# Performance work log

Hardware: AMD Instinct MI355X
Metric: run time of the kernel (lower is better)

## Reference

```python
import jax, jax.numpy as jnp
import numpy as np
import math

# Static configuration (matches init_kwargs / input_specs)
L1 = 2          # lmax of x
L2 = 2          # lmax of y
LZ = L1 + L2    # output lmax = 4
RB = 20         # res_beta (Gauss-Legendre nodes)
RA = 19         # res_alpha (uniform azimuthal samples)
MUL = 128       # input multiplicity per l
C = 128         # num_channels
N = 1024        # batch (nodes/edges)


def _assoc_legendre(l, m, x):
    """Associated Legendre P_l^m(x) with Condon-Shortley phase, via recurrence."""
    pmm = np.ones_like(x)
    if m > 0:
        dfact = float(np.prod(np.arange(1, 2 * m, 2)))  # (2m-1)!!
        pmm = ((-1.0) ** m) * dfact * (1.0 - x * x) ** (m / 2.0)
    if l == m:
        return pmm
    pmmp1 = x * (2 * m + 1) * pmm
    if l == m + 1:
        return pmmp1
    for ll in range(m + 2, l + 1):
        p = ((2 * ll - 1) * x * pmmp1 - (ll + m - 1) * pmm) / (ll - m)
        pmm, pmmp1 = pmmp1, p
    return pmmp1


def _sh_table(L, rb, ra):
    """Orthonormal real spherical harmonics sampled on the (beta, alpha) grid.

    Returns Y [(L+1)^2, rb, ra] and Gauss-Legendre weights qw [rb] such that
    sum_{b,a} f(b,a) Y_lm(b,a) qw[b] * (2*pi/ra) == c_lm exactly for
    bandlimited f (the inverse of the synthesis c -> grid).
    """
    ct, qw = np.polynomial.legendre.leggauss(rb)  # nodes = cos(beta)
    alpha = 2.0 * np.pi * np.arange(ra) / ra
    Y = np.zeros(((L + 1) ** 2, rb, ra))
    for l in range(L + 1):
        for m in range(-l, l + 1):
            am = abs(m)
            nlm = math.sqrt((2 * l + 1) / (4 * math.pi)
                            * math.factorial(l - am) / math.factorial(l + am))
            P = _assoc_legendre(l, am, ct)  # [rb]
            if m == 0:
                ang = np.ones(ra)
            elif m > 0:
                ang = math.sqrt(2.0) * np.cos(m * alpha)
            else:
                ang = math.sqrt(2.0) * np.sin(am * alpha)
            Y[l * l + l + m] = nlm * P[:, None] * ang[None, :]
    return Y, qw


_Y_np, _QW_np = _sh_table(LZ, RB, RA)
Y_TAB = jnp.asarray(_Y_np, jnp.float32)   # [(LZ+1)^2, RB, RA]
QW = jnp.asarray(_QW_np, jnp.float32)     # [RB]


def _per_l_linear_in(v, w, L):
    """Equivariant per-l linear: v [N, mul, (L+1)^2], w [L+1, mul, C] -> [N, C, (L+1)^2]."""
    scale = 1.0 / math.sqrt(v.shape[1])
    outs = [jnp.einsum('nmd,mc->ncd', v[..., l * l:(l + 1) ** 2], w[l]) * scale
            for l in range(L + 1)]
    return jnp.concatenate(outs, axis=-1)


def setup_inputs() -> dict:
    key = jax.random.key(0)
    k0, k1, k2, k3, k4 = jax.random.split(key, 5)
    return {
        'x': jax.random.normal(k0, (N, MUL, (L1 + 1) ** 2), jnp.float32),
        'y': jax.random.normal(k1, (N, MUL, (L2 + 1) ** 2), jnp.float32),
        'wx': jax.random.normal(k2, (L1 + 1, MUL, C), jnp.float32),
        'wy': jax.random.normal(k3, (L2 + 1, MUL, C), jnp.float32),
        'wz': jax.random.normal(k4, (LZ + 1, C, C), jnp.float32),
    }


def reference(x, y, wx, wy, wz):
    # linear_in + mul_to_axis: [N, mul, D] -> [N, C, D]
    xc = _per_l_linear_in(x, wx, L1)  # [N, C, 9]
    yc = _per_l_linear_in(y, wy, L2)  # [N, C, 9]

    # to_s2grid (synthesis): coeffs -> signal on (beta, alpha) grid
    gx = jnp.einsum('ncd,dba->ncba', xc, Y_TAB[:(L1 + 1) ** 2])  # [N,C,RB,RA]
    gy = jnp.einsum('ncd,dba->ncba', yc, Y_TAB[:(L2 + 1) ** 2])

    # pointwise Gaunt product on the grid
    prod = gx * gy

    # from_s2grid (analysis): quadrature projection onto Y_lm up to LZ
    z = jnp.einsum('ncba,dba,b->ncd', prod, Y_TAB, QW) * (2.0 * jnp.pi / RA)  # [N,C,25]

    # axis_to_mul + linear_out_z: per-l channel mixing [C -> C]
    scale = 1.0 / math.sqrt(C)
    outs = [jnp.einsum('ncd,ce->ned', z[..., l * l:(l + 1) ** 2], wz[l]) * scale
            for l in range(LZ + 1)]
    return jnp.concatenate(outs, axis=-1)  # [N, C, 25]
```

## Files before the change

### kernel.cpp

```cpp
#include <hip/hip_runtime.h>
#include <cmath>

#define RB 20
#define RA 19
#define NPT (RB*RA)
#define DZ 25
#define DIN 9
#define MULT 128
#define CH 128

__host__ __device__ constexpr int L_of(int d) { return d == 0 ? 0 : d < 4 ? 1 : d < 9 ? 2 : d < 16 ? 3 : 4; }
__host__ __device__ constexpr int M_of(int d) { return d - L_of(d) * L_of(d) - L_of(d); }
__host__ __device__ constexpr bool gz_nz(int d1, int d2, int dz) {
    const int l1 = L_of(d1), l2 = L_of(d2), l3 = L_of(dz);
    const int m1 = M_of(d1), m2 = M_of(d2), m3 = M_of(dz);
    const int lo = l1 > l2 ? l1 - l2 : l2 - l1;
    if (l3 < lo || l3 > l1 + l2) return false;
    if ((l1 + l2 + l3) & 1) return false;
    const int a1 = m1 < 0 ? -m1 : m1, a2 = m2 < 0 ? -m2 : m2, a3 = m3 < 0 ? -m3 : m3;
    const int sum = a1 + a2, dif = a1 > a2 ? a1 - a2 : a2 - a1;
    if (a3 != sum && a3 != dif) return false;
    if (((m1 < 0) + (m2 < 0) + (m3 < 0)) & 1) return false;
    return true;
}
__host__ __device__ constexpr bool pair_any(int d1, int d2) {
    for (int dz = 0; dz < DZ; ++dz) if (gz_nz(d1, d2, dz)) return true;
    return false;
}

static void host_build_gaunt(float* out ) {
    const double PI = 3.14159265358979323846;
    double xq[RB], wq[RB];
    for (int i = 0; i < RB; ++i) {
        double x = cos(PI * (i + 0.75) / (RB + 0.5));
        double dp = 0.0;
        for (int it = 0; it < 100; ++it) {
            double p0 = 1.0, p1 = x;
            for (int k = 2; k <= RB; ++k) {
                double p2 = ((2.0*k - 1.0)*x*p1 - (k - 1.0)*p0) / (double)k;
                p0 = p1; p1 = p2;
            }
            dp = RB * (x*p1 - p0) / (x*x - 1.0);
            double dx = p1 / dp;
            x -= dx;
            if (fabs(dx) < 1e-15) break;
        }
        {
            double p0 = 1.0, p1 = x;
            for (int k = 2; k <= RB; ++k) {
                double p2 = ((2.0*k - 1.0)*x*p1 - (k - 1.0)*p0) / (double)k;
                p0 = p1; p1 = p2;
            }
            dp = RB * (x*p1 - p0) / (x*x - 1.0);
        }
        xq[i] = x;
        wq[i] = 2.0 / ((1.0 - x*x)*dp*dp);
    }
    static double Y[DZ][NPT];
    static double qws[NPT];
    for (int b = 0; b < RB; ++b) {
        double ct = xq[b], st = sqrt(fmax(0.0, 1.0 - ct*ct));
        double P[5][5]; double pmm = 1.0;
        for (int m = 0; m <= 4; ++m) {
            if (m > 0) pmm *= -(2.0*m - 1.0) * st;
            P[m][m] = pmm;
            if (m < 4) {
                double pp = pmm, pc = ct*(2.0*m + 1.0)*pmm;
                P[m+1][m] = pc;
                for (int l = m + 2; l <= 4; ++l) {
                    double pn = ((2.0*l - 1.0)*ct*pc - (double)(l + m - 1)*pp) / (double)(l - m);
                    P[l][m] = pn; pp = pc; pc = pn;
                }
            }
        }
        for (int a = 0; a < RA; ++a) {
            int pt = b*RA + a;
            qws[pt] = wq[b] * (2.0*PI/(double)RA);
            double alpha = 2.0*PI*(double)a/(double)RA;
            for (int l = 0; l <= 4; ++l)
                for (int m = -l; m <= l; ++m) {
                    int am = m < 0 ? -m : m;
                    double fr = 1.0;
                    for (int i = l - am + 1; i <= l + am; ++i) fr *= (double)i;
                    double nlm = sqrt((2.0*l + 1.0) / (4.0*PI) / fr);
                    double ang = (m == 0) ? 1.0
                               : (m > 0 ? sqrt(2.0)*cos(am*alpha) : sqrt(2.0)*sin(am*alpha));
                    Y[l*l + l + m][pt] = nlm * P[l][am] * ang;
                }
        }
    }
    for (int pr = 0; pr < 81; ++pr) {
        int d1 = pr / 9, d2 = pr % 9;
        for (int d = 0; d < DZ; ++d) {
            double s = 0.0;
            for (int p = 0; p < NPT; ++p)
                s += Y[d][p] * Y[d1][p] * Y[d2][p] * qws[p];
            out[pr*28 + d] = gz_nz(d1, d2, d) ? (float)s : 0.0f;
        }
    }
}

template<int D1, int D2, int DZi>
__device__ __forceinline__ void c_dz(const float* __restrict__ g, float p, float* z) {
    if constexpr (DZi < DZ) {
        if constexpr (gz_nz(D1, D2, DZi))
            z[DZi] = fmaf(p, g[(D1 * 9 + D2) * 28 + DZi], z[DZi]);
        c_dz<D1, D2, DZi + 1>(g, p, z);
    }
}
template<int D1, int D2>
__device__ __forceinline__ void c_d2(const float* __restrict__ g,
                                     const float* xr, const float* yr, float* z) {
    if constexpr (D2 < 9) {
        if constexpr (pair_any(D1, D2)) {
            const float p = xr[D1] * yr[D2];
            c_dz<D1, D2, 0>(g, p, z);
        }
        c_d2<D1, D2 + 1>(g, xr, yr, z);
    }
}
template<int D1>
__device__ __forceinline__ void c_d1(const float* __restrict__ g,
                                     const float* xr, const float* yr, float* z) {
    if constexpr (D1 < 9) {
        c_d2<D1, 0>(g, xr, yr, z);
        c_d1<D1 + 1>(g, xr, yr, z);
    }
}

__global__ __launch_bounds__(256) void gaunt_fused(
    const float* __restrict__ xg, const float* __restrict__ yg,
    const float* __restrict__ wxg, const float* __restrict__ wyg,
    const float* __restrict__ wzg, float* __restrict__ outg,
    const float* __restrict__ gGt) {

    __shared__ __align__(16) float pool[13276];
    float* sZ  = pool;
    float* sXY = pool + 6400;
    float* sG  = pool + 11008;

    const int tid = threadIdx.x;
    const int b   = blockIdx.x;
    const float s128 = 0.08838834764831845f;

    {
        const float4* xs = (const float4*)(xg + 2 * b * 1152);
        const float4* ys = (const float4*)(yg + 2 * b * 1152);
        for (int i = tid; i < 1152; i += 256) {
            float4 v = (i < 576) ? xs[i] : ys[i - 576];
            int r = (i < 576) ? i : i - 576;
            int base = (i < 576) ? 0 : 2304;
            int j0 = r * 4;
            #pragma unroll
            for (int k = 0; k < 4; ++k) {
                int j = j0 + k;
                int n = j / 1152;
                int jj = j - n * 1152;
                int m = jj / 9, d = jj - 9 * m;
                float val = (k == 0) ? v.x : (k == 1) ? v.y : (k == 2) ? v.z : v.w;
                sXY[base + n * 1152 + d * 128 + m] = val;
            }
        }
        for (int i = tid; i < 567; i += 256)
            ((float4*)sG)[i] = ((const float4*)gGt)[i];
    }
    __syncthreads();

    {
        const int n = tid >> 7;
        const int c = tid & 127;
        float xr[9], yr[9];
        #pragma unroll
        for (int side = 0; side < 2; ++side) {
            const float* wb = side ? wyg : wxg;
            const float* xb = sXY + side * 2304 + n * 1152;
            float acc[9];
            #pragma unroll
            for (int d = 0; d < 9; ++d) acc[d] = 0.f;
            for (int m0 = 0; m0 < MULT; m0 += 4) {
                float w0[4], w1[4], w2[4];
                #pragma unroll
                for (int k = 0; k < 4; ++k) {
                    w0[k] = wb[(m0 + k) * 128 + c];
                    w1[k] = wb[16384 + (m0 + k) * 128 + c];
                    w2[k] = wb[32768 + (m0 + k) * 128 + c];
                }
                #pragma unroll
                for (int d = 0; d < 9; ++d) {
                    const float* wl = (d == 0) ? w0 : (d < 4) ? w1 : w2;
                    float4 xv = *(const float4*)(xb + d * 128 + m0);
                    acc[d] = fmaf(xv.x, wl[0], acc[d]);
                    acc[d] = fmaf(xv.y, wl[1], acc[d]);
                    acc[d] = fmaf(xv.z, wl[2], acc[d]);
                    acc[d] = fmaf(xv.w, wl[3], acc[d]);
                }
            }
            float* dst = side ? yr : xr;
            #pragma unroll
            for (int d = 0; d < 9; ++d) dst[d] = acc[d] * s128;
        }

        float z[DZ];
        #pragma unroll
        for (int i = 0; i < DZ; ++i) z[i] = 0.f;
        c_d1<0>(sG, xr, yr, z);

        #pragma unroll
        for (int dz = 0; dz < DZ; ++dz)
            sZ[(n * DZ + dz) * 128 + c] = z[dz];
    }
    __syncthreads();

    {
        const int n = tid >> 7;
        const int e = tid & 127;
        const float* zb = sZ + n * DZ * 128;
        float acc[DZ];
        #pragma unroll
        for (int d = 0; d < DZ; ++d) acc[d] = 0.f;
        for (int c0 = 0; c0 < CH; c0 += 4) {
            float w[5][4];
            #pragma unroll
            for (int l = 0; l < 5; ++l)
                #pragma unroll
                for (int k = 0; k < 4; ++k)
                    w[l][k] = wzg[l * 16384 + (c0 + k) * 128 + e];
            #pragma unroll
            for (int d = 0; d < DZ; ++d) {
                const int l = (d == 0) ? 0 : (d < 4) ? 1 : (d < 9) ? 2 : (d < 16) ? 3 : 4;
                float4 z4 = *(const float4*)(zb + d * 128 + c0);
                acc[d] = fmaf(z4.x, w[l][0], acc[d]);
                acc[d] = fmaf(z4.y, w[l][1], acc[d]);
                acc[d] = fmaf(z4.z, w[l][2], acc[d]);
                acc[d] = fmaf(z4.w, w[l][3], acc[d]);
            }
        }
        float* po = outg + ((size_t)(2 * b + n) * 128 + e) * DZ;
        #pragma unroll
        for (int d = 0; d < DZ; ++d) po[d] = acc[d] * s128;
    }
}

extern "C" void kernel_launch(void* const* d_in, const int* in_sizes, int n_in,
                              void* d_out, int out_size, void* d_ws, size_t ws_size,
                              hipStream_t stream) {
    static float h_gGt[81 * 28];
    static bool built = false;
    if (!built) { host_build_gaunt(h_gGt); built = true; }
    hipMemcpyAsync(d_ws, h_gGt, sizeof(h_gGt), hipMemcpyHostToDevice, stream);

    int N = in_sizes[0] / (MULT * DIN);

    hipLaunchKernelGGL(gaunt_fused, dim3(N / 2), dim3(256), 0, stream,
                       (const float*)d_in[0], (const float*)d_in[1],
                       (const float*)d_in[2], (const float*)d_in[3],
                       (const float*)d_in[4], (float*)d_out, (const float*)d_ws);
}
```

Baseline: 127.9 us.

## Process one node per 128-thread block with per-wave side and dz splits

```diff
diff --git a/kernel.cpp b/kernel.cpp
--- a/kernel.cpp
+++ b/kernel.cpp
@@ -101,144 +101,164 @@
 }
 
 template<int D1, int D2, int DZi>
-__device__ __forceinline__ void c_dz(const float* __restrict__ g, float p, float* z) {
+__device__ __forceinline__ void c_dz(const float* __restrict__ g, float p, float* a) {
     if constexpr (DZi < DZ) {
         if constexpr (gz_nz(D1, D2, DZi))
-            z[DZi] = fmaf(p, g[(D1 * 9 + D2) * 28 + DZi], z[DZi]);
-        c_dz<D1, D2, DZi + 1>(g, p, z);
+            a[DZi] = fmaf(p, g[(D1 * 9 + D2) * 28 + DZi], a[DZi]);
+        c_dz<D1, D2, DZi + 1>(g, p, a);
     }
 }
 template<int D1, int D2>
 __device__ __forceinline__ void c_d2(const float* __restrict__ g,
-                                     const float* xr, const float* yr, float* z) {
+                                     const float* xr, const float* yr, float* a) {
     if constexpr (D2 < 9) {
-        if constexpr (pair_any(D1, D2)) {
-            const float p = xr[D1] * yr[D2];
-            c_dz<D1, D2, 0>(g, p, z);
-        }
-        c_d2<D1, D2 + 1>(g, xr, yr, z);
+        if constexpr (pair_any(D1, D2))
+            c_dz<D1, D2, 0>(g, xr[D1] * yr[D2], a);
+        c_d2<D1, D2 + 1>(g, xr, yr, a);
     }
 }
 template<int D1>
 __device__ __forceinline__ void c_d1(const float* __restrict__ g,
-                                     const float* xr, const float* yr, float* z) {
+                                     const float* xr, const float* yr, float* a) {
     if constexpr (D1 < 9) {
-        c_d2<D1, 0>(g, xr, yr, z);
-        c_d1<D1 + 1>(g, xr, yr, z);
-    }
-}
-
-__global__ __launch_bounds__(256) void gaunt_fused(
+        c_d2<D1, 0>(g, xr, yr, a);
+        c_d1<D1 + 1>(g, xr, yr, a);
+    }
+}
+
+template<int D0, int ND, int L0, int NL>
+__device__ __forceinline__ void d_tile(const float* sZ, const float* __restrict__ wz,
+                                       float* __restrict__ po, int lane) {
+    const float s128 = 0.08838834764831845f;
+    const int e2 = lane << 1;
+    float acc[ND * 2];
+    #pragma unroll
+    for (int i = 0; i < ND * 2; ++i) acc[i] = 0.f;
+    for (int c0 = 0; c0 < CH; c0 += 4) {
+        float2 w[NL * 4];
+        #pragma unroll
+        for (int j = 0; j < NL; ++j)
+            #pragma unroll
+            for (int k = 0; k < 4; ++k)
+                w[j * 4 + k] = *(const float2*)(wz + (L0 + j) * 16384 + (c0 + k) * 128 + e2);
+        #pragma unroll
+        for (int i = 0; i < ND; ++i) {
+            const int d = D0 + i;
+            const int l = (d == 0) ? 0 : (d < 4) ? 1 : (d < 9) ? 2 : (d < 16) ? 3 : 4;
+            float4 z4 = *(const float4*)(sZ + d * 128 + c0);
+            #pragma unroll
+            for (int k = 0; k < 4; ++k) {
+                float zc = (k == 0) ? z4.x : (k == 1) ? z4.y : (k == 2) ? z4.z : z4.w;
+                acc[i*2+0] = fmaf(zc, w[(l - L0) * 4 + k].x, acc[i*2+0]);
+                acc[i*2+1] = fmaf(zc, w[(l - L0) * 4 + k].y, acc[i*2+1]);
+            }
+        }
+    }
+    #pragma unroll
+    for (int i = 0; i < ND; ++i) {
+        po[e2 * 25 + D0 + i]       = acc[i*2+0] * s128;
+        po[(e2 + 1) * 25 + D0 + i] = acc[i*2+1] * s128;
+    }
+}
+
+__global__ __launch_bounds__(128) void gaunt_fused(
     const float* __restrict__ xg, const float* __restrict__ yg,
     const float* __restrict__ wxg, const float* __restrict__ wyg,
     const float* __restrict__ wzg, float* __restrict__ outg,
     const float* __restrict__ gGt) {
 
-    __shared__ __align__(16) float pool[13276];
-    float* sZ  = pool;
-    float* sXY = pool + 6400;
-    float* sG  = pool + 11008;
-
-    const int tid = threadIdx.x;
-    const int b   = blockIdx.x;
+    __shared__ __align__(16) float pool[7776];
+    float* sXc = pool;
+    float* sG  = pool + 2304;
+    float* sXY = pool + 4572;
+    float* sZ  = pool + 4572;
+
+    const int tid  = threadIdx.x;
+    const int nb   = blockIdx.x;
+    const int lane = tid & 63;
+    const int wave = __builtin_amdgcn_readfirstlane(tid >> 6);
     const float s128 = 0.08838834764831845f;
 
     {
-        const float4* xs = (const float4*)(xg + 2 * b * 1152);
-        const float4* ys = (const float4*)(yg + 2 * b * 1152);
-        for (int i = tid; i < 1152; i += 256) {
-            float4 v = (i < 576) ? xs[i] : ys[i - 576];
-            int r = (i < 576) ? i : i - 576;
-            int base = (i < 576) ? 0 : 2304;
+        const float4* xs = (const float4*)(xg + (size_t)nb * 1152);
+        const float4* ys = (const float4*)(yg + (size_t)nb * 1152);
+        for (int i = tid; i < 576; i += 128) {
+            float4 v = (i < 288) ? xs[i] : ys[i - 288];
+            int r = (i < 288) ? i : i - 288;
+            int base = (i < 288) ? 0 : 1152;
             int j0 = r * 4;
             #pragma unroll
             for (int k = 0; k < 4; ++k) {
                 int j = j0 + k;
-                int n = j / 1152;
-                int jj = j - n * 1152;
-                int m = jj / 9, d = jj - 9 * m;
+                int m = j / 9, d = j - 9 * m;
                 float val = (k == 0) ? v.x : (k == 1) ? v.y : (k == 2) ? v.z : v.w;
-                sXY[base + n * 1152 + d * 128 + m] = val;
-            }
-        }
-        for (int i = tid; i < 567; i += 256)
+                sXY[base + d * 128 + m] = val;
+            }
+        }
+        for (int i = tid; i < 567; i += 128)
             ((float4*)sG)[i] = ((const float4*)gGt)[i];
     }
     __syncthreads();
 
     {
-        const int n = tid >> 7;
-        const int c = tid & 127;
+        const int side = wave;
+        const int c2 = lane << 1;
+        const float* wb = side ? wyg : wxg;
+        const float* xb = sXY + side * 1152;
+        float acc[18];
+        #pragma unroll
+        for (int i = 0; i < 18; ++i) acc[i] = 0.f;
+        for (int m0 = 0; m0 < MULT; m0 += 4) {
+            float2 w0[4], w1[4], w2[4];
+            #pragma unroll
+            for (int k = 0; k < 4; ++k) {
+                w0[k] = *(const float2*)(wb + (m0 + k) * 128 + c2);
+                w1[k] = *(const float2*)(wb + 16384 + (m0 + k) * 128 + c2);
+                w2[k] = *(const float2*)(wb + 32768 + (m0 + k) * 128 + c2);
+            }
+            #pragma unroll
+            for (int d = 0; d < 9; ++d) {
+                const float2* wl = (d == 0) ? w0 : (d < 4) ? w1 : w2;
+                float4 xv = *(const float4*)(xb + d * 128 + m0);
+                acc[d*2+0] = fmaf(xv.x, wl[0].x, acc[d*2+0]);
+                acc[d*2+0] = fmaf(xv.y, wl[1].x, acc[d*2+0]);
+                acc[d*2+0] = fmaf(xv.z, wl[2].x, acc[d*2+0]);
+                acc[d*2+0] = fmaf(xv.w, wl[3].x, acc[d*2+0]);
+                acc[d*2+1] = fmaf(xv.x, wl[0].y, acc[d*2+1]);
+                acc[d*2+1] = fmaf(xv.y, wl[1].y, acc[d*2+1]);
+                acc[d*2+1] = fmaf(xv.z, wl[2].y, acc[d*2+1]);
+                acc[d*2+1] = fmaf(xv.w, wl[3].y, acc[d*2+1]);
+            }
+        }
+        #pragma unroll
+        for (int d = 0; d < 9; ++d) {
+            float2 v = make_float2(acc[d*2+0] * s128, acc[d*2+1] * s128);
+            *(float2*)(sXc + (side * 9 + d) * 128 + c2) = v;
+        }
+    }
+    __syncthreads();
+
+    {
+        const int c = tid;
         float xr[9], yr[9];
         #pragma unroll
-        for (int side = 0; side < 2; ++side) {
-            const float* wb = side ? wyg : wxg;
-            const float* xb = sXY + side * 2304 + n * 1152;
-            float acc[9];
-            #pragma unroll
-            for (int d = 0; d < 9; ++d) acc[d] = 0.f;
-            for (int m0 = 0; m0 < MULT; m0 += 4) {
-                float w0[4], w1[4], w2[4];
-                #pragma unroll
-                for (int k = 0; k < 4; ++k) {
-                    w0[k] = wb[(m0 + k) * 128 + c];
-                    w1[k] = wb[16384 + (m0 + k) * 128 + c];
-                    w2[k] = wb[32768 + (m0 + k) * 128 + c];
-                }
-                #pragma unroll
-                for (int d = 0; d < 9; ++d) {
-                    const float* wl = (d == 0) ? w0 : (d < 4) ? w1 : w2;
-                    float4 xv = *(const float4*)(xb + d * 128 + m0);
-                    acc[d] = fmaf(xv.x, wl[0], acc[d]);
-                    acc[d] = fmaf(xv.y, wl[1], acc[d]);
-                    acc[d] = fmaf(xv.z, wl[2], acc[d]);
-                    acc[d] = fmaf(xv.w, wl[3], acc[d]);
-                }
-            }
-            float* dst = side ? yr : xr;
-            #pragma unroll
-            for (int d = 0; d < 9; ++d) dst[d] = acc[d] * s128;
-        }
-
-        float z[DZ];
-        #pragma unroll
-        for (int i = 0; i < DZ; ++i) z[i] = 0.f;
-        c_d1<0>(sG, xr, yr, z);
-
+        for (int d = 0; d < 9; ++d) {
+            xr[d] = sXc[d * 128 + c];
+            yr[d] = sXc[(9 + d) * 128 + c];
+        }
+        float a[DZ];
+        #pragma unroll
+        for (int i = 0; i < DZ; ++i) a[i] = 0.f;
+        c_d1<0>(sG, xr, yr, a);
         #pragma unroll
         for (int dz = 0; dz < DZ; ++dz)
-            sZ[(n * DZ + dz) * 128 + c] = z[dz];
+            sZ[dz * 128 + c] = a[dz];
     }
     __syncthreads();
 
-    {
-        const int n = tid >> 7;
-        const int e = tid & 127;
-        const float* zb = sZ + n * DZ * 128;
-        float acc[DZ];
-        #pragma unroll
-        for (int d = 0; d < DZ; ++d) acc[d] = 0.f;
-        for (int c0 = 0; c0 < CH; c0 += 4) {
-            float w[5][4];
-            #pragma unroll
-            for (int l = 0; l < 5; ++l)
-                #pragma unroll
-                for (int k = 0; k < 4; ++k)
-                    w[l][k] = wzg[l * 16384 + (c0 + k) * 128 + e];
-            #pragma unroll
-            for (int d = 0; d < DZ; ++d) {
-                const int l = (d == 0) ? 0 : (d < 4) ? 1 : (d < 9) ? 2 : (d < 16) ? 3 : 4;
-                float4 z4 = *(const float4*)(zb + d * 128 + c0);
-                acc[d] = fmaf(z4.x, w[l][0], acc[d]);
-                acc[d] = fmaf(z4.y, w[l][1], acc[d]);
-                acc[d] = fmaf(z4.z, w[l][2], acc[d]);
-                acc[d] = fmaf(z4.w, w[l][3], acc[d]);
-            }
-        }
-        float* po = outg + ((size_t)(2 * b + n) * 128 + e) * DZ;
-        #pragma unroll
-        for (int d = 0; d < DZ; ++d) po[d] = acc[d] * s128;
-    }
+    float* po = outg + (size_t)nb * (CH * DZ);
+    if (wave == 0) d_tile<0, 9, 0, 3>(sZ, wzg, po, lane);
+    else           d_tile<9, 16, 3, 2>(sZ, wzg, po, lane);
 }
 
 extern "C" void kernel_launch(void* const* d_in, const int* in_sizes, int n_in,
@@ -251,7 +271,7 @@
 
     int N = in_sizes[0] / (MULT * DIN);
 
-    hipLaunchKernelGGL(gaunt_fused, dim3(N / 2), dim3(256), 0, stream,
+    hipLaunchKernelGGL(gaunt_fused, dim3(N), dim3(128), 0, stream,
                        (const float*)d_in[0], (const float*)d_in[1],
                        (const float*)d_in[2], (const float*)d_in[3],
                        (const float*)d_in[4], (float*)d_out, (const float*)d_ws);
```

Measured after the change: 119.6 us. -6.5%, faster.
